# Optimization experiments

Hardware: AMD Instinct MI355X
Metric: run time of the kernel (lower is better)

Reference implementation:

```python
import jax, jax.numpy as jnp
import numpy as np

HIDDEN = 256
PA = 32          # pairwise_attention_size
PW = 64          # pairwise_size
B, L = 4, 512


def setup_inputs() -> dict:
    key = jax.random.key(0)
    k1, k2, k3, k4, k5, k6 = jax.random.split(key, 6)
    s_in = 1.0 / np.sqrt(HIDDEN)
    s_out = 1.0 / np.sqrt(PA * PA)
    return {
        "hidden_states": jax.random.normal(k1, (B, L, HIDDEN), dtype=jnp.float32),
        "pairwise_states": jax.random.normal(k2, (B, L, L, PW), dtype=jnp.float32),
        "W_in": jax.random.uniform(k3, (PA, HIDDEN), jnp.float32, -s_in, s_in),
        "b_in": jax.random.uniform(k4, (PA,), jnp.float32, -s_in, s_in),
        "W_out": jax.random.uniform(k5, (PW, PA * PA), jnp.float32, -s_out, s_out),
        "b_out": jax.random.uniform(k6, (PW,), jnp.float32, -s_out, s_out),
    }


def reference(hidden_states, pairwise_states, W_in, b_in, W_out, b_out):
    # in_proj: [B, L, H] -> [B, L, PA]
    h = jnp.einsum("blh,ph->blp", hidden_states, W_in) + b_in
    # Original math: triangle[b,i,j,p,q] = h[b,j,p] * h[b,i,q], flattened (p major)
    # then out_proj. Algebraically reorder to avoid the [B,L,L,PA^2] intermediate:
    # out[b,i,j,o] = sum_{p,q} W_out[o, p*PA+q] * h[b,j,p] * h[b,i,q] + b_out[o]
    Wr = W_out.reshape(W_out.shape[0], PA, PA)  # [O, p, q]
    t = jnp.einsum("bjp,opq->bjoq", h, Wr)       # small: [B, L, O, PA]
    out = jnp.einsum("bjoq,biq->bijo", t, h) + b_out
    return out + pairwise_states
```

## Files before the change

kernel.cpp:

```cpp
#include <hip/hip_runtime.h>

#define BB  4
#define LL  512
#define HID 256
#define PAi 32
#define OO  64

using bf16x8 = __attribute__((ext_vector_type(8))) short;
using f32x4  = __attribute__((ext_vector_type(4))) float;

__device__ inline ushort f2bf(float x) {
    union { float f; unsigned u; } v; v.f = x;
    unsigned r = (v.u + 0x7fff + ((v.u >> 16) & 1)) >> 16;
    return (ushort)r;
}

__device__ inline void barrier_lds() {
    asm volatile("s_waitcnt lgkmcnt(0)" ::: "memory");
    __builtin_amdgcn_s_barrier();
}

__global__ __launch_bounds__(256) void k_in(const float* __restrict__ hidden,
                                            const float* __restrict__ W_in,
                                            const float* __restrict__ b_in,
                                            float* __restrict__ h,
                                            ushort* __restrict__ hb) {
    __shared__ float4 hid[8 * 64];
    const int tid  = threadIdx.x;
    const int row0 = blockIdx.x * 8;
    const float4* src = (const float4*)(hidden + (size_t)row0 * HID);
    hid[tid]       = src[tid];
    hid[tid + 256] = src[tid + 256];
    __syncthreads();
    const int p = tid & 31;
    const int r = tid >> 5;
    const float4* w = (const float4*)(W_in + (size_t)p * HID);
    float acc = 0.f;
#pragma unroll
    for (int k = 0; k < 64; ++k) {
        float4 hv = hid[r * 64 + k];
        float4 wv = w[k];
        acc += hv.x * wv.x + hv.y * wv.y + hv.z * wv.z + hv.w * wv.w;
    }
    const float val = acc + b_in[p];
    h[(size_t)(row0 + r) * PAi + p]  = val;
    hb[(size_t)(row0 + r) * PAi + p] = f2bf(val);
}

#define RMID 16
__global__ __launch_bounds__(256) void k_mid(const float* __restrict__ h,
                                             const float* __restrict__ W_out,
                                             ushort* __restrict__ t) {
    __shared__ __attribute__((aligned(16))) float hst[PAi][RMID];
    const int tid  = threadIdx.x;
    const int row0 = blockIdx.x * RMID;
    for (int s = tid; s < RMID * PAi; s += 256) {
        const int r = s >> 5, p = s & 31;
        hst[p][r] = h[(size_t)(row0 + r) * PAi + p];
    }
    __syncthreads();
    const int qg = tid & 7;
    const int o1 = tid >> 3;
    const float4* W4 = (const float4*)W_out;
    float4 accA[RMID], accB[RMID];
#pragma unroll
    for (int r = 0; r < RMID; ++r) {
        accA[r] = float4{0, 0, 0, 0};
        accB[r] = float4{0, 0, 0, 0};
    }
#pragma unroll 2
    for (int p = 0; p < PAi; ++p) {
        const float4 wa = W4[(o1 * PAi + p) * 8 + qg];
        const float4 wb = W4[((o1 + 32) * PAi + p) * 8 + qg];
#pragma unroll
        for (int r4 = 0; r4 < RMID / 4; ++r4) {
            const float4 h4 = *(const float4*)&hst[p][r4 * 4];
            const float hr[4] = {h4.x, h4.y, h4.z, h4.w};
#pragma unroll
            for (int e = 0; e < 4; ++e) {
                const int r = r4 * 4 + e;
                accA[r].x += hr[e] * wa.x; accA[r].y += hr[e] * wa.y;
                accA[r].z += hr[e] * wa.z; accA[r].w += hr[e] * wa.w;
                accB[r].x += hr[e] * wb.x; accB[r].y += hr[e] * wb.y;
                accB[r].z += hr[e] * wb.z; accB[r].w += hr[e] * wb.w;
            }
        }
    }
#pragma unroll
    for (int r = 0; r < RMID; ++r) {
        ushort4 ua, ub;
        ua.x = f2bf(accA[r].x); ua.y = f2bf(accA[r].y); ua.z = f2bf(accA[r].z); ua.w = f2bf(accA[r].w);
        ub.x = f2bf(accB[r].x); ub.y = f2bf(accB[r].y); ub.z = f2bf(accB[r].z); ub.w = f2bf(accB[r].w);
        ushort* dst = t + (size_t)(row0 + r) * OO * PAi;
        *(ushort4*)(dst + (o1 * 8 + qg) * 4)        = ua;
        *(ushort4*)(dst + ((o1 + 32) * 8 + qg) * 4) = ub;
    }
}

#define SEG  4096
#define CH   256
#define NCH  (SEG / CH)
#define LSTR 260
__global__ __launch_bounds__(256, 2) void k_out(const ushort* __restrict__ t,
                                                const ushort* __restrict__ hb,
                                                const float* __restrict__ pw,
                                                const float* __restrict__ b_out,
                                                float* __restrict__ out) {
    __shared__ float sA[16 * LSTR];
    __shared__ float sB[16 * LSTR];
    const int tid  = threadIdx.x;
    const int lane = tid & 63;
    const int wave = tid >> 6;
    const int b    = blockIdx.z;
    const int i0   = blockIdx.y * 32;
    const int seg0 = blockIdx.x * SEG;
    const int l15  = lane & 15;
    const int g    = lane >> 4;

    const bf16x8 hf0 = *(const bf16x8*)(hb + ((size_t)(b * LL + i0 + l15)) * PAi + g * 8);
    const bf16x8 hf1 = *(const bf16x8*)(hb + ((size_t)(b * LL + i0 + 16 + l15)) * PAi + g * 8);
    const f32x4 bo4 = *(const f32x4*)(b_out + ((lane * 4) & 63));
    const size_t outrow0 = ((size_t)(b * LL + i0)) * (LL * OO);

    auto loadT = [&](int c, bf16x8* tf) {
        const ushort* tb0 = t + ((size_t)b * LL * OO + seg0 + c * CH + wave * 64 + l15) * PAi + g * 8;
#pragma unroll
        for (int tt = 0; tt < 4; ++tt)
            tf[tt] = *(const bf16x8*)(tb0 + (size_t)tt * (16 * PAi));
    };
    auto loadP = [&](int c, f32x4* pv) {
        const int cbase = seg0 + c * CH;
#pragma unroll
        for (int it = 0; it < 2; ++it)
#pragma unroll
            for (int rr = 0; rr < 4; ++rr)
                pv[it * 4 + rr] = *(const f32x4*)(pw + outrow0 +
                    (size_t)(it * 16 + wave * 4 + rr) * (LL * OO) + cbase + lane * 4);
    };
    auto mfmaS = [&](const bf16x8* tf, const bf16x8 hfi, float* sbuf) {
#pragma unroll
        for (int tt = 0; tt < 4; ++tt) {
            f32x4 z = {0.f, 0.f, 0.f, 0.f};
            f32x4 a = __builtin_amdgcn_mfma_f32_16x16x32_bf16(tf[tt], hfi, z, 0, 0, 0);
            *(f32x4*)&sbuf[l15 * LSTR + wave * 64 + tt * 16 + g * 4] = a;
        }
    };
    auto cons = [&](int c, int it, const f32x4* pv4, const float* sbuf) {
        const int cbase = seg0 + c * CH;
#pragma unroll
        for (int rr = 0; rr < 4; ++rr) {
            const f32x4 a4 = *(const f32x4*)&sbuf[(wave * 4 + rr) * LSTR + lane * 4];
            f32x4 res = a4 + bo4 + pv4[rr];
            __builtin_nontemporal_store(res, (f32x4*)(out + outrow0 +
                (size_t)(it * 16 + wave * 4 + rr) * (LL * OO) + cbase + lane * 4));
        }
    };

    bf16x8 tf0[4], tf1[4];
    f32x4  pv0[8], pv1[8];

    loadT(0, tf0); loadP(0, pv0);

    for (int c = 0; c < NCH; c += 2) {
        loadT(c + 1, tf1); loadP(c + 1, pv1);
        mfmaS(tf0, hf0, sA);
        barrier_lds();
        mfmaS(tf0, hf1, sB);
        cons(c, 0, pv0, sA);
        barrier_lds();
        cons(c, 1, pv0 + 4, sB);
        if (c + 2 < NCH) { loadT(c + 2, tf0); loadP(c + 2, pv0); }
        mfmaS(tf1, hf0, sA);
        barrier_lds();
        mfmaS(tf1, hf1, sB);
        cons(c + 1, 0, pv1, sA);
        barrier_lds();
        cons(c + 1, 1, pv1 + 4, sB);
    }
}

extern "C" void kernel_launch(void* const* d_in, const int* in_sizes, int n_in,
                              void* d_out, int out_size, void* d_ws, size_t ws_size,
                              hipStream_t stream) {
    const float* hidden = (const float*)d_in[0];
    const float* pw     = (const float*)d_in[1];
    const float* W_in   = (const float*)d_in[2];
    const float* b_in   = (const float*)d_in[3];
    const float* W_out  = (const float*)d_in[4];
    const float* b_out  = (const float*)d_in[5];
    float* out = (float*)d_out;

    float*  h  = (float*)d_ws;
    ushort* hb = (ushort*)(h + (size_t)BB * LL * PAi);
    ushort* tb = hb + (size_t)BB * LL * PAi;

    k_in <<<dim3(BB * LL / 8), 256, 0, stream>>>(hidden, W_in, b_in, h, hb);
    k_mid<<<dim3(BB * LL / RMID), 256, 0, stream>>>(h, W_out, tb);
    k_out<<<dim3(LL * OO / SEG, LL / 32, BB), 256, 0, stream>>>(tb, hb, pw, b_out, out);
}
```

Baseline: 125.8 us.

## Make k_out blocks own a j-o column and stream over all i rows

Each k_out block now holds a fixed 256-wide slice of the t operand in registers for its whole life and loops over all 512 i rows in 16-row steps, loading only the small h fragment per step. The old blocks handled a 32-row i tile over a 4096-wide j-o segment and reloaded t per chunk. This cuts redundant t loads and reduces the grid from 512 to 512 blocks of a different shape. The trade-off is a longer serial loop per block and a different memory access pattern for the pairwise reads and output writes, which are now strided by full rows.

```diff
diff --git a/kernel.cpp b/kernel.cpp
--- a/kernel.cpp
+++ b/kernel.cpp
@@ -97,9 +97,8 @@
     }
 }
 
-#define SEG  4096
-#define CH   256
-#define NCH  (SEG / CH)
+#define WJO  256
+#define NIT  (LL / 16)
 #define LSTR 260
 __global__ __launch_bounds__(256, 2) void k_out(const ushort* __restrict__ t,
                                                 const ushort* __restrict__ hb,
@@ -111,33 +110,30 @@
     const int tid  = threadIdx.x;
     const int lane = tid & 63;
     const int wave = tid >> 6;
-    const int b    = blockIdx.z;
-    const int i0   = blockIdx.y * 32;
-    const int seg0 = blockIdx.x * SEG;
+    const int b    = blockIdx.y;
+    const int jo0  = blockIdx.x * WJO;
     const int l15  = lane & 15;
     const int g    = lane >> 4;
 
-    const bf16x8 hf0 = *(const bf16x8*)(hb + ((size_t)(b * LL + i0 + l15)) * PAi + g * 8);
-    const bf16x8 hf1 = *(const bf16x8*)(hb + ((size_t)(b * LL + i0 + 16 + l15)) * PAi + g * 8);
-    const f32x4 bo4 = *(const f32x4*)(b_out + ((lane * 4) & 63));
-    const size_t outrow0 = ((size_t)(b * LL + i0)) * (LL * OO);
-
-    auto loadT = [&](int c, bf16x8* tf) {
-        const ushort* tb0 = t + ((size_t)b * LL * OO + seg0 + c * CH + wave * 64 + l15) * PAi + g * 8;
+    bf16x8 tf[4];
+    {
+        const ushort* tb0 = t + ((size_t)b * LL * OO + jo0 + wave * 64 + l15) * PAi + g * 8;
 #pragma unroll
         for (int tt = 0; tt < 4; ++tt)
             tf[tt] = *(const bf16x8*)(tb0 + (size_t)tt * (16 * PAi));
+    }
+    const f32x4 bo4 = *(const f32x4*)(b_out + ((lane * 4) & 63));
+
+    auto loadH = [&](int it) -> bf16x8 {
+        return *(const bf16x8*)(hb + ((size_t)(b * LL + it * 16 + l15)) * PAi + g * 8);
     };
-    auto loadP = [&](int c, f32x4* pv) {
-        const int cbase = seg0 + c * CH;
+    auto loadP = [&](int it, f32x4* pv) {
 #pragma unroll
-        for (int it = 0; it < 2; ++it)
-#pragma unroll
-            for (int rr = 0; rr < 4; ++rr)
-                pv[it * 4 + rr] = *(const f32x4*)(pw + outrow0 +
-                    (size_t)(it * 16 + wave * 4 + rr) * (LL * OO) + cbase + lane * 4);
+        for (int rr = 0; rr < 4; ++rr)
+            pv[rr] = *(const f32x4*)(pw + ((size_t)(b * LL + it * 16 + wave * 4 + rr)) * (LL * OO)
+                                       + jo0 + lane * 4);
     };
-    auto mfmaS = [&](const bf16x8* tf, const bf16x8 hfi, float* sbuf) {
+    auto mfmaS = [&](const bf16x8 hfi, float* sbuf) {
 #pragma unroll
         for (int tt = 0; tt < 4; ++tt) {
             f32x4 z = {0.f, 0.f, 0.f, 0.f};
@@ -145,37 +141,33 @@
             *(f32x4*)&sbuf[l15 * LSTR + wave * 64 + tt * 16 + g * 4] = a;
         }
     };
-    auto cons = [&](int c, int it, const f32x4* pv4, const float* sbuf) {
-        const int cbase = seg0 + c * CH;
+    auto cons = [&](int it, const f32x4* pv, const float* sbuf) {
 #pragma unroll
         for (int rr = 0; rr < 4; ++rr) {
             const f32x4 a4 = *(const f32x4*)&sbuf[(wave * 4 + rr) * LSTR + lane * 4];
-            f32x4 res = a4 + bo4 + pv4[rr];
-            __builtin_nontemporal_store(res, (f32x4*)(out + outrow0 +
-                (size_t)(it * 16 + wave * 4 + rr) * (LL * OO) + cbase + lane * 4));
+            f32x4 res = a4 + bo4 + pv[rr];
+            __builtin_nontemporal_store(res,
+                (f32x4*)(out + ((size_t)(b * LL + it * 16 + wave * 4 + rr)) * (LL * OO)
+                             + jo0 + lane * 4));
         }
     };
 
-    bf16x8 tf0[4], tf1[4];
-    f32x4  pv0[8], pv1[8];
+    bf16x8 hfA = loadH(0), hfB = loadH(1);
+    f32x4  pvA[4], pvB[4];
+    loadP(0, pvA); loadP(1, pvB);
 
-    loadT(0, tf0); loadP(0, pv0);
+    mfmaS(hfA, sA);
+    barrier_lds();
 
-    for (int c = 0; c < NCH; c += 2) {
-        loadT(c + 1, tf1); loadP(c + 1, pv1);
-        mfmaS(tf0, hf0, sA);
+    for (int k = 0; k < NIT; k += 2) {
+        mfmaS(hfB, sB);
+        cons(k, pvA, sA);
+        if (k + 2 < NIT) { hfA = loadH(k + 2); loadP(k + 2, pvA); }
         barrier_lds();
-        mfmaS(tf0, hf1, sB);
-        cons(c, 0, pv0, sA);
+        if (k + 2 < NIT) mfmaS(hfA, sA);
+        cons(k + 1, pvB, sB);
+        if (k + 3 < NIT) { hfB = loadH(k + 3); loadP(k + 3, pvB); }
         barrier_lds();
-        cons(c, 1, pv0 + 4, sB);
-        if (c + 2 < NCH) { loadT(c + 2, tf0); loadP(c + 2, pv0); }
-        mfmaS(tf1, hf0, sA);
-        barrier_lds();
-        mfmaS(tf1, hf1, sB);
-        cons(c + 1, 0, pv1, sA);
-        barrier_lds();
-        cons(c + 1, 1, pv1 + 4, sB);
     }
 }
 
@@ -196,5 +188,5 @@
 
     k_in <<<dim3(BB * LL / 8), 256, 0, stream>>>(hidden, W_in, b_in, h, hb);
     k_mid<<<dim3(BB * LL / RMID), 256, 0, stream>>>(h, W_out, tb);
-    k_out<<<dim3(LL * OO / SEG, LL / 32, BB), 256, 0, stream>>>(tb, hb, pw, b_out, out);
+    k_out<<<dim3(LL * OO / WJO, BB), 256, 0, stream>>>(tb, hb, pw, b_out, out);
 }
```

New measurement: 113.4 us. 9.9% less time.
